# Optimization experiments

Measured on AMD Instinct MI355X. Metric: run time of the kernel, lower is better.

Reference implementation:

```python
import jax, jax.numpy as jnp
import numpy as np


def _chain_edges(n):
    # bidirectional chain edges + self loops (PyG GATConv add_self_loops=True default)
    src = np.concatenate([np.arange(n - 1), np.arange(1, n), np.arange(n)])
    dst = np.concatenate([np.arange(1, n), np.arange(n - 1), np.arange(n)])
    return jnp.asarray(src), jnp.asarray(dst)


def _gat(x, W, a_src, a_dst, bias, src, dst, n, heads, ch, concat):
    # x: [B, n, Fin]; PyG GATConv v1 math (lin has no bias, bias added post-agg)
    B = x.shape[0]
    xh = (x @ W).reshape(B, n, heads, ch)  # [B,n,h,c]
    es = jnp.einsum('bnhc,hc->bnh', xh, a_src)
    ed = jnp.einsum('bnhc,hc->bnh', xh, a_dst)
    e = jax.nn.leaky_relu(es[:, src] + ed[:, dst], 0.2)  # [B,E,h]
    e = jnp.moveaxis(e, 1, 0)                            # [E,B,h]
    m = jax.ops.segment_max(e, dst, num_segments=n)      # scatter-softmax over incoming edges
    w = jnp.exp(e - m[dst])
    denom = jax.ops.segment_sum(w, dst, num_segments=n)
    alpha = w / denom[dst]                               # [E,B,h]
    msgs = alpha[..., None] * jnp.moveaxis(xh[:, src], 1, 0)  # [E,B,h,c]
    out = jnp.moveaxis(jax.ops.segment_sum(msgs, dst, num_segments=n), 0, 1)  # [B,n,h,c]
    out = out.reshape(B, n, heads * ch) if concat else out.mean(axis=2)
    return out + bias


def _mlp(x, w1, b1, w2, b2, w3, b3):
    h = jax.nn.leaky_relu(x @ w1 + b1, 0.01)
    h = jax.nn.leaky_relu(h @ w2 + b2, 0.01)
    return h @ w3 + b3


def setup_inputs() -> dict:
    key = jax.random.key(0)
    ks = jax.random.split(key, 21)
    B, n, d_state, hid, da = 2048, 50, 64, 128, 4
    r = lambda k, shp, s: (jax.random.normal(k, shp, dtype=jnp.float32) * s)
    return {
        'state': r(ks[0], (B, n, d_state), 1.0),
        'W1': r(ks[1], (d_state, 2 * hid), 0.1), 'att_src1': r(ks[2], (2, hid), 0.1),
        'att_dst1': r(ks[3], (2, hid), 0.1), 'b1': r(ks[4], (2 * hid,), 0.02),
        'W2': r(ks[5], (2 * hid, hid), 0.1), 'att_src2': r(ks[6], (1, hid), 0.1),
        'att_dst2': r(ks[7], (1, hid), 0.1), 'b2': r(ks[8], (hid,), 0.02),
        'aw1': r(ks[9], (hid, 128), 0.1), 'ab1': r(ks[10], (128,), 0.02),
        'aw2': r(ks[11], (128, 128), 0.1), 'ab2': r(ks[12], (128,), 0.02),
        'aw3': r(ks[13], (128, da), 0.1), 'ab3': r(ks[14], (da,), 0.02),
        'vw1': r(ks[15], (hid, 128), 0.1), 'vb1': r(ks[16], (128,), 0.02),
        'vw2': r(ks[17], (128, 128), 0.1), 'vb2': r(ks[18], (128,), 0.02),
        'vw3': r(ks[19], (128, 1), 0.1), 'vb3': r(ks[20], (1,), 0.02),
    }


def reference(state, W1, att_src1, att_dst1, b1, W2, att_src2, att_dst2, b2,
              aw1, ab1, aw2, ab2, aw3, ab3, vw1, vb1, vw2, vb2, vw3, vb3):
    B, n, _ = state.shape
    src, dst = _chain_edges(n)
    x = jax.nn.gelu(_gat(state, W1, att_src1, att_dst1, b1, src, dst, n, 2, 128, True), approximate=False)
    x = jax.nn.gelu(_gat(x, W2, att_src2, att_dst2, b2, src, dst, n, 1, 128, False), approximate=False)
    graph_emb = x.mean(axis=1)                      # global_mean_pool over chain nodes
    value = _mlp(graph_emb, vw1, vb1, vw2, vb2, vw3, vb3)   # [B,1]
    mean = _mlp(x, aw1, ab1, aw2, ab2, aw3, ab3).reshape(B, -1)  # [B, n*d_action]
    return mean, value
```

## Files before the change

kernel.cpp:

```cpp
#include <hip/hip_runtime.h>

#define DI __device__ __forceinline__

typedef unsigned int uint32;
typedef unsigned short u16;
typedef __attribute__((ext_vector_type(8))) short s8v;
typedef __attribute__((ext_vector_type(4))) float f4v;

DI float lrelu(float x, float s){ return x > 0.f ? x : s*x; }
DI float fastrcp(float x){ float r; asm("v_rcp_f32 %0, %1" : "=v"(r) : "v"(x)); return r; }
DI u16 f2bu(float f){ uint32 u = __float_as_uint(f); return (u16)((u + 0x7FFFu + ((u>>16)&1u)) >> 16); }
DI float b16f(u16 u){ return __uint_as_float(((uint32)u)<<16); }

DI float gelu_f(float x){
  const float z = fabsf(x) * 0.70710678118654752f;
  const float t = fastrcp(1.f + 0.3275911f*z);
  float p = 1.061405429f;
  p = p*t - 1.453152027f;
  p = p*t + 1.421413741f;
  p = p*t - 0.284496736f;
  p = p*t + 0.254829592f;
  p = p*t;
  const float e = __expf(-z*z);
  float er = 1.f - p*e;
  er = copysignf(er, x);
  return 0.5f*x*(1.f + er);
}

DI f4v mfma16(s8v a, s8v b, f4v c){
  return __builtin_amdgcn_mfma_f32_16x16x32_bf16(a, b, c, 0, 0, 0);
}

constexpr int NNODE = 50;
constexpr int NT = 512;
constexpr int SCS = 134;

constexpr int WS1  = 0;
constexpr int WS2  = 18432;
constexpr int WSA1 = 55296;
constexpr int WSA2 = 71680;
constexpr int WSA3 = 88064;
constexpr int WSTOT= 90112;
constexpr int X2OFF= 90112;

__global__ __launch_bounds__(256)
void ac_prep(const float* __restrict__ w1, const float* __restrict__ as1, const float* __restrict__ ad1,
             const float* __restrict__ w2, const float* __restrict__ as2, const float* __restrict__ ad2,
             const float* __restrict__ aw1, const float* __restrict__ aw2, const float* __restrict__ aw3,
             u16* __restrict__ ws)
{
  const int T1 = 2*144*64, T2 = 144*256, T3 = 128*128;
  for (int t = blockIdx.x*blockDim.x + threadIdx.x; t < WSTOT; t += gridDim.x*blockDim.x){
    float v; int o;
    if (t < T1){
      int h = t / 9216, r = t - h*9216, n = r>>6, k = r&63;
      if (n < 128) v = w1[k*256 + h*128 + n];
      else if (n < 130){
        const float* av = ((n==129) ? ad1 : as1) + h*128;
        const float* wr = w1 + k*256 + h*128;
        float s = 0.f;
        for (int c=0;c<128;++c) s += wr[c]*av[c];
        v = s;
      } else v = 0.f;
      o = WS1 + h*9216 + n*64 + k;
    } else if (t < T1+T2){
      int j = t - T1, n = j>>8, k = j&255;
      if (n < 128) v = w2[k*128 + n];
      else if (n < 130){
        const float* av = (n==129) ? ad2 : as2;
        const float* wr = w2 + k*128;
        float s = 0.f;
        for (int c=0;c<128;++c) s += wr[c]*av[c];
        v = s;
      } else v = 0.f;
      o = WS2 + n*256 + k;
    } else if (t < T1+T2+T3){
      int j = t - T1 - T2, n = j>>7, k = j&127;
      v = aw1[k*128 + n];
      o = WSA1 + n*128 + k;
    } else if (t < T1+T2+2*T3){
      int j = t - T1 - T2 - T3, n = j>>7, k = j&127;
      v = aw2[k*128 + n];
      o = WSA2 + n*128 + k;
    } else {
      int j = t - T1 - T2 - 2*T3, m = j>>7, k = j&127;
      v = (m < 4) ? aw3[k*4 + m] : 0.f;
      o = WSA3 + m*128 + k;
    }
    ws[o] = f2bu(v);
  }
}

__global__ __launch_bounds__(NT)
void ac_gat(const float* __restrict__ state,
            const float* __restrict__ b1, const float* __restrict__ b2,
            u16* __restrict__ ws)
{
  __shared__ __align__(16) float sm[13100];
  u16*   pAb = (u16*)sm;
  u16*   pAs = (u16*)sm;
  float* sc  = sm + 6400;

  const int tid = threadIdx.x, b = blockIdx.x;
  const int wid = tid>>6, l15 = tid&15, g = (tid>>4)&3;

  {
    const float4* xb4 = (const float4*)(state + (size_t)b * (NNODE*64));
    for (int t = tid; t < 800; t += NT){
      float4 v = xb4[t];
      int i = t>>4, k0 = (t&15)*4;
      ushort4 u;
      u.x = f2bu(v.x); u.y = f2bu(v.y); u.z = f2bu(v.z); u.w = f2bu(v.w);
      *(ushort4*)(pAs + i*64 + (k0 ^ ((i&7)<<3))) = u;
    }
  }
  __syncthreads();

  s8v aS[4][2];
  #pragma unroll
  for (int mt=0;mt<4;++mt)
    #pragma unroll
    for (int ks=0;ks<2;++ks){
      int row = mt*16 + l15, c = ks*32 + g*8;
      aS[mt][ks] = *(const s8v*)(pAs + row*64 + (c ^ ((row&7)<<3)));
    }

  for (int h=0; h<2; ++h){
    for (int nt = wid; nt < 9; nt += 8){
      f4v acc[4];
      #pragma unroll
      for (int mt=0;mt<4;++mt) acc[mt] = (f4v){0.f,0.f,0.f,0.f};
      #pragma unroll
      for (int ks=0;ks<2;++ks){
        s8v bf = *(const s8v*)(ws + WS1 + h*9216 + (nt*16 + l15)*64 + ks*32 + g*8);
        #pragma unroll
        for (int mt=0;mt<4;++mt) acc[mt] = mfma16(aS[mt][ks], bf, acc[mt]);
      }
      const int col = nt*16 + l15;
      if (col < 130){
        #pragma unroll
        for (int mt=0;mt<4;++mt){
          #pragma unroll
          for (int r=0;r<4;++r){
            const int row = mt*16 + g*4 + r;
            if (mt < 3 || row < NNODE) sc[row*SCS + col] = acc[mt][r];
          }
        }
      }
    }
    __syncthreads();

    {
      const int i = tid & 63;
      if (i < NNODE){
        const float edi = sc[i*SCS + 129];
        const float eS = __expf(lrelu(sc[i*SCS + 128] + edi, 0.2f));
        const float eL = (i > 0)       ? __expf(lrelu(sc[(i-1)*SCS + 128] + edi, 0.2f)) : 0.f;
        const float eR = (i < NNODE-1) ? __expf(lrelu(sc[(i+1)*SCS + 128] + edi, 0.2f)) : 0.f;
        const float rs = fastrcp(eL + eS + eR);
        sc[i*SCS + 130] = eL*rs;
        sc[i*SCS + 131] = eS*rs;
        sc[i*SCS + 132] = eR*rs;
      }
    }
    {
      const int q = tid>>7, j = tid&127, jj = h*128 + j;
      const int i0 = q*13, i1 = (i0+13 < NNODE) ? i0+13 : NNODE;
      const float bj = b1[jj];
      float pv  = (i0 > 0) ? sc[(i0-1)*SCS + j] : 0.f;
      float cur = sc[i0*SCS + j];
      #pragma unroll 4
      for (int i = i0; i < i1; ++i){
        const float nx = (i < NNODE-1) ? sc[(i+1)*SCS + j] : 0.f;
        const float wL = sc[i*SCS + 130], wS = sc[i*SCS + 131], wR = sc[i*SCS + 132];
        const float v = gelu_f(wL*pv + wS*cur + wR*nx + bj);
        pAb[i*256 + (jj ^ ((i&7)<<3))] = f2bu(v);
        pv = cur; cur = nx;
      }
    }
    __syncthreads();
  }

  for (int nt = wid; nt < 9; nt += 8){
    f4v acc[4];
    #pragma unroll
    for (int mt=0;mt<4;++mt) acc[mt] = (f4v){0.f,0.f,0.f,0.f};
    #pragma unroll
    for (int ks=0;ks<8;++ks){
      s8v bf = *(const s8v*)(ws + WS2 + (nt*16 + l15)*256 + ks*32 + g*8);
      #pragma unroll
      for (int mt=0;mt<4;++mt){
        const int row = mt*16 + l15, c = ks*32 + g*8;
        s8v a = *(const s8v*)(pAb + row*256 + (c ^ ((row&7)<<3)));
        acc[mt] = mfma16(a, bf, acc[mt]);
      }
    }
    const int col = nt*16 + l15;
    if (col < 130){
      #pragma unroll
      for (int mt=0;mt<4;++mt){
        #pragma unroll
        for (int r=0;r<4;++r){
          const int row = mt*16 + g*4 + r;
          if (mt < 3 || row < NNODE) sc[row*SCS + col] = acc[mt][r];
        }
      }
    }
  }
  __syncthreads();

  {
    const int i = tid & 63;
    if (i < NNODE){
      const float edi = sc[i*SCS + 129];
      const float eS = __expf(lrelu(sc[i*SCS + 128] + edi, 0.2f));
      const float eL = (i > 0)       ? __expf(lrelu(sc[(i-1)*SCS + 128] + edi, 0.2f)) : 0.f;
      const float eR = (i < NNODE-1) ? __expf(lrelu(sc[(i+1)*SCS + 128] + edi, 0.2f)) : 0.f;
      const float rs = fastrcp(eL + eS + eR);
      sc[i*SCS + 130] = eL*rs;
      sc[i*SCS + 131] = eS*rs;
      sc[i*SCS + 132] = eR*rs;
    }
  }
  {
    u16* x2g = ws + X2OFF + (size_t)b * (NNODE*128);
    const int q = tid>>7, j = tid&127;
    const int i0 = q*13, i1 = (i0+13 < NNODE) ? i0+13 : NNODE;
    const float bj = b2[j];
    float pv  = (i0 > 0) ? sc[(i0-1)*SCS + j] : 0.f;
    float cur = sc[i0*SCS + j];
    #pragma unroll 4
    for (int i = i0; i < i1; ++i){
      const float nx = (i < NNODE-1) ? sc[(i+1)*SCS + j] : 0.f;
      const float wL = sc[i*SCS + 130], wS = sc[i*SCS + 131], wR = sc[i*SCS + 132];
      const float v = gelu_f(wL*pv + wS*cur + wR*nx + bj);
      x2g[i*128 + j] = f2bu(v);
      pv = cur; cur = nx;
    }
  }
}

__global__ __launch_bounds__(NT)
void ac_head(const u16* __restrict__ ws,
             const float* __restrict__ ab1, const float* __restrict__ ab2,
             const float* __restrict__ ab3, float* __restrict__ out_mean, int headM)
{
  __shared__ __align__(16) float sm[8192];
  u16* xt = (u16*)sm;
  u16* a4 = (u16*)(sm + 4096);

  const int tid = threadIdx.x, bid = blockIdx.x;
  const int wid = tid>>6, l15 = tid&15, g = (tid>>4)&3;

  {
    const int row = tid>>3, c0 = (tid&7)*16;
    const int grow = bid*64 + row;
    if (grow < headM){
      const uint4* src = (const uint4*)(ws + X2OFF + (size_t)grow*128 + c0);
      uint4 v0 = src[0], v1 = src[1];
      *(uint4*)(xt + row*128 + ( c0      ^ ((row&7)<<3))) = v0;
      *(uint4*)(xt + row*128 + ((c0 + 8) ^ ((row&7)<<3))) = v1;
    }
  }
  __syncthreads();

  {
    const int nt = wid;
    f4v acc[4];
    #pragma unroll
    for (int mt=0;mt<4;++mt) acc[mt] = (f4v){0.f,0.f,0.f,0.f};
    #pragma unroll
    for (int ks=0;ks<4;++ks){
      s8v bf = *(const s8v*)(ws + WSA1 + (nt*16 + l15)*128 + ks*32 + g*8);
      #pragma unroll
      for (int mt=0;mt<4;++mt){
        const int row = mt*16 + l15, c = ks*32 + g*8;
        s8v a = *(const s8v*)(xt + row*128 + (c ^ ((row&7)<<3)));
        acc[mt] = mfma16(a, bf, acc[mt]);
      }
    }
    const int col = nt*16 + l15;
    const float bj = ab1[col];
    #pragma unroll
    for (int mt=0;mt<4;++mt)
      #pragma unroll
      for (int r=0;r<4;++r){
        const int row = mt*16 + g*4 + r;
        a4[row*128 + (col ^ ((row&7)<<3))] = f2bu(lrelu(acc[mt][r] + bj, 0.01f));
      }
  }
  __syncthreads();

  {
    const int nt = wid;
    f4v acc[4];
    #pragma unroll
    for (int mt=0;mt<4;++mt) acc[mt] = (f4v){0.f,0.f,0.f,0.f};
    #pragma unroll
    for (int ks=0;ks<4;++ks){
      s8v bf = *(const s8v*)(ws + WSA2 + (nt*16 + l15)*128 + ks*32 + g*8);
      #pragma unroll
      for (int mt=0;mt<4;++mt){
        const int row = mt*16 + l15, c = ks*32 + g*8;
        s8v a = *(const s8v*)(a4 + row*128 + (c ^ ((row&7)<<3)));
        acc[mt] = mfma16(a, bf, acc[mt]);
      }
    }
    const int col = nt*16 + l15;
    const float bj = ab2[col];
    #pragma unroll
    for (int mt=0;mt<4;++mt)
      #pragma unroll
      for (int r=0;r<4;++r){
        const int row = mt*16 + g*4 + r;
        xt[row*128 + (col ^ ((row&7)<<3))] = f2bu(lrelu(acc[mt][r] + bj, 0.01f));
      }
  }
  __syncthreads();

  if (wid < 4){
    const int mt = wid;
    f4v acc = (f4v){0.f,0.f,0.f,0.f};
    #pragma unroll
    for (int ks=0;ks<4;++ks){
      s8v bf = *(const s8v*)(ws + WSA3 + l15*128 + ks*32 + g*8);
      const int row = mt*16 + l15, c = ks*32 + g*8;
      s8v a = *(const s8v*)(xt + row*128 + (c ^ ((row&7)<<3)));
      acc = mfma16(a, bf, acc);
    }
    if (l15 < 4){
      const float bj = ab3[l15];
      #pragma unroll
      for (int r=0;r<4;++r){
        const int grow = bid*64 + mt*16 + g*4 + r;
        if (grow < headM) out_mean[(size_t)grow*4 + l15] = acc[r] + bj;
      }
    }
  }
}

__global__ __launch_bounds__(NT)
void ac_value(const u16* __restrict__ ws,
              const float* __restrict__ vw1, const float* __restrict__ vb1,
              const float* __restrict__ vw2, const float* __restrict__ vb2,
              const float* __restrict__ vw3, const float* __restrict__ vb3,
              float* __restrict__ out_val, int B)
{
  __shared__ float gs[8*128];
  __shared__ float vs[8*128];
  const int tid = threadIdx.x, wid = tid>>6, j = tid&63;
  const int b = blockIdx.x*8 + wid;
  if (b >= B) return;
  const u16* xb = ws + X2OFF + (size_t)b * (NNODE*128);

  float g0 = 0.f, g1 = 0.f;
  for (int i=0;i<NNODE;++i){
    g0 += b16f(xb[i*128 + j]);
    g1 += b16f(xb[i*128 + 64 + j]);
  }
  gs[wid*128 + j]      = g0 * 0.02f;
  gs[wid*128 + 64 + j] = g1 * 0.02f;
  asm volatile("s_waitcnt lgkmcnt(0)" ::: "memory");
  __builtin_amdgcn_sched_barrier(0);

  float a0=0.f, a1=0.f;
  #pragma unroll 4
  for (int k=0;k<128;++k){
    const float gk = gs[wid*128 + k];
    a0 += gk*vw1[k*128 + j];
    a1 += gk*vw1[k*128 + j + 64];
  }
  vs[wid*128 + j]      = lrelu(a0 + vb1[j],    0.01f);
  vs[wid*128 + 64 + j] = lrelu(a1 + vb1[j+64], 0.01f);
  asm volatile("s_waitcnt lgkmcnt(0)" ::: "memory");
  __builtin_amdgcn_sched_barrier(0);

  float c0=0.f, c1=0.f;
  #pragma unroll 4
  for (int k=0;k<128;++k){
    const float hk = vs[wid*128 + k];
    c0 += hk*vw2[k*128 + j];
    c1 += hk*vw2[k*128 + j + 64];
  }
  const float va = lrelu(c0 + vb2[j],    0.01f);
  const float vb = lrelu(c1 + vb2[j+64], 0.01f);
  float p = va*vw3[j] + vb*vw3[j+64];
  #pragma unroll
  for (int off=32; off>0; off>>=1) p += __shfl_down(p, off);
  if (j == 0) out_val[b] = p + vb3[0];
}

__global__ __launch_bounds__(NT)
void ac_main(const float* __restrict__ state,
             const float* __restrict__ b1, const float* __restrict__ b2,
             const float* __restrict__ ab1, const float* __restrict__ ab2,
             const float* __restrict__ ab3,
             const float* __restrict__ vw1, const float* __restrict__ vb1,
             const float* __restrict__ vw2, const float* __restrict__ vb2,
             const float* __restrict__ vw3, const float* __restrict__ vb3,
             const u16* __restrict__ ws,
             float* __restrict__ out_mean, float* __restrict__ out_val)
{
  __shared__ __align__(16) float sm[13228];
  u16*   pAb  = (u16*)sm;
  u16*   pAs  = (u16*)sm;
  float* gebP = sm + 3200;
  float* vh1  = sm + 3712;
  float* sc   = sm + 6400;
  u16*   pAb2 = (u16*)(sm + 6400);
  float* geb  = sm + 13100;

  const int tid = threadIdx.x, b = blockIdx.x;
  const int wid = tid>>6, l15 = tid&15, g = (tid>>4)&3;

  {
    const float4* xb4 = (const float4*)(state + (size_t)b * (NNODE*64));
    for (int t = tid; t < 800; t += NT){
      float4 v = xb4[t];
      int i = t>>4, k0 = (t&15)*4;
      ushort4 u;
      u.x = f2bu(v.x); u.y = f2bu(v.y); u.z = f2bu(v.z); u.w = f2bu(v.w);
      *(ushort4*)(pAs + i*64 + (k0 ^ ((i&7)<<3))) = u;
    }
  }
  __syncthreads();

  s8v aS[4][2];
  #pragma unroll
  for (int mt=0;mt<4;++mt)
    #pragma unroll
    for (int ks=0;ks<2;++ks){
      int row = mt*16 + l15, c = ks*32 + g*8;
      aS[mt][ks] = *(const s8v*)(pAs + row*64 + (c ^ ((row&7)<<3)));
    }

  for (int h=0; h<2; ++h){
    for (int nt = wid; nt < 9; nt += 8){
      f4v acc[4];
      #pragma unroll
      for (int mt=0;mt<4;++mt) acc[mt] = (f4v){0.f,0.f,0.f,0.f};
      #pragma unroll
      for (int ks=0;ks<2;++ks){
        s8v bf = *(const s8v*)(ws + WS1 + h*9216 + (nt*16 + l15)*64 + ks*32 + g*8);
        #pragma unroll
        for (int mt=0;mt<4;++mt) acc[mt] = mfma16(aS[mt][ks], bf, acc[mt]);
      }
      const int col = nt*16 + l15;
      if (col < 130){
        #pragma unroll
        for (int mt=0;mt<4;++mt){
          #pragma unroll
          for (int r=0;r<4;++r){
            const int row = mt*16 + g*4 + r;
            if (mt < 3 || row < NNODE) sc[row*SCS + col] = acc[mt][r];
          }
        }
      }
    }
    __syncthreads();
    {
      const int i = tid & 63;
      if (i < NNODE){
        const float edi = sc[i*SCS + 129];
        const float eS = __expf(lrelu(sc[i*SCS + 128] + edi, 0.2f));
        const float eL = (i > 0)       ? __expf(lrelu(sc[(i-1)*SCS + 128] + edi, 0.2f)) : 0.f;
        const float eR = (i < NNODE-1) ? __expf(lrelu(sc[(i+1)*SCS + 128] + edi, 0.2f)) : 0.f;
        const float rs = fastrcp(eL + eS + eR);
        sc[i*SCS + 130] = eL*rs;
        sc[i*SCS + 131] = eS*rs;
        sc[i*SCS + 132] = eR*rs;
      }
    }
    {
      const int q = tid>>7, j = tid&127, jj = h*128 + j;
      const int i0 = q*13, i1 = (i0+13 < NNODE) ? i0+13 : NNODE;
      const float bj = b1[jj];
      float pv  = (i0 > 0) ? sc[(i0-1)*SCS + j] : 0.f;
      float cur = sc[i0*SCS + j];
      #pragma unroll 4
      for (int i = i0; i < i1; ++i){
        const float nx = (i < NNODE-1) ? sc[(i+1)*SCS + j] : 0.f;
        const float wL = sc[i*SCS + 130], wS = sc[i*SCS + 131], wR = sc[i*SCS + 132];
        const float v = gelu_f(wL*pv + wS*cur + wR*nx + bj);
        pAb[i*256 + (jj ^ ((i&7)<<3))] = f2bu(v);
        pv = cur; cur = nx;
      }
    }
    __syncthreads();
  }

  for (int nt = wid; nt < 9; nt += 8){
    f4v acc[4];
    #pragma unroll
    for (int mt=0;mt<4;++mt) acc[mt] = (f4v){0.f,0.f,0.f,0.f};
    #pragma unroll
    for (int ks=0;ks<8;++ks){
      s8v bf = *(const s8v*)(ws + WS2 + (nt*16 + l15)*256 + ks*32 + g*8);
      #pragma unroll
      for (int mt=0;mt<4;++mt){
        const int row = mt*16 + l15, c = ks*32 + g*8;
        s8v a = *(const s8v*)(pAb + row*256 + (c ^ ((row&7)<<3)));
        acc[mt] = mfma16(a, bf, acc[mt]);
      }
    }
    const int col = nt*16 + l15;
    if (col < 130){
      #pragma unroll
      for (int mt=0;mt<4;++mt){
        #pragma unroll
        for (int r=0;r<4;++r){
          const int row = mt*16 + g*4 + r;
          if (mt < 3 || row < NNODE) sc[row*SCS + col] = acc[mt][r];
        }
      }
    }
  }
  __syncthreads();

  {
    const int i = tid & 63;
    if (i < NNODE){
      const float edi = sc[i*SCS + 129];
      const float eS = __expf(lrelu(sc[i*SCS + 128] + edi, 0.2f));
      const float eL = (i > 0)       ? __expf(lrelu(sc[(i-1)*SCS + 128] + edi, 0.2f)) : 0.f;
      const float eR = (i < NNODE-1) ? __expf(lrelu(sc[(i+1)*SCS + 128] + edi, 0.2f)) : 0.f;
      const float rs = fastrcp(eL + eS + eR);
      sc[i*SCS + 130] = eL*rs;
      sc[i*SCS + 131] = eS*rs;
      sc[i*SCS + 132] = eR*rs;
    }
  }
  {
    const int q = tid>>7, j = tid&127;
    const int i0 = q*13, i1 = (i0+13 < NNODE) ? i0+13 : NNODE;
    const float bj = b2[j];
    float ps = 0.f;
    float pv  = (i0 > 0) ? sc[(i0-1)*SCS + j] : 0.f;
    float cur = sc[i0*SCS + j];
    #pragma unroll 4
    for (int i = i0; i < i1; ++i){
      const float nx = (i < NNODE-1) ? sc[(i+1)*SCS + j] : 0.f;
      const float wL = sc[i*SCS + 130], wS = sc[i*SCS + 131], wR = sc[i*SCS + 132];
      const float v = gelu_f(wL*pv + wS*cur + wR*nx + bj);
      pAb[i*128 + (j ^ ((i&7)<<3))] = f2bu(v);
      ps += v;
      pv = cur; cur = nx;
    }
    gebP[q*128 + j] = ps;
  }
  __syncthreads();

  {
    const int nt = wid;
    f4v acc[4];
    #pragma unroll
    for (int mt=0;mt<4;++mt) acc[mt] = (f4v){0.f,0.f,0.f,0.f};
    #pragma unroll
    for (int ks=0;ks<4;++ks){
      s8v bf = *(const s8v*)(ws + WSA1 + (nt*16 + l15)*128 + ks*32 + g*8);
      #pragma unroll
      for (int mt=0;mt<4;++mt){
        const int row = mt*16 + l15, c = ks*32 + g*8;
        s8v a = *(const s8v*)(pAb + row*128 + (c ^ ((row&7)<<3)));
        acc[mt] = mfma16(a, bf, acc[mt]);
      }
    }
    const int col = nt*16 + l15;
    const float bj = ab1[col];
    #pragma unroll
    for (int mt=0;mt<4;++mt){
      #pragma unroll
      for (int r=0;r<4;++r){
        const int row = mt*16 + g*4 + r;
        if (mt < 3 || row < NNODE){
          const float v = lrelu(acc[mt][r] + bj, 0.01f);
          pAb2[row*128 + (col ^ ((row&7)<<3))] = f2bu(v);
        }
      }
    }
    if (tid < 128)
      geb[tid] = (gebP[tid] + gebP[128+tid] + gebP[256+tid] + gebP[384+tid]) * 0.02f;
  }
  __syncthreads();

  {
    const int nt = wid;
    f4v acc[4];
    #pragma unroll
    for (int mt=0;mt<4;++mt) acc[mt] = (f4v){0.f,0.f,0.f,0.f};
    #pragma unroll
    for (int ks=0;ks<4;++ks){
      s8v bf = *(const s8v*)(ws + WSA2 + (nt*16 + l15)*128 + ks*32 + g*8);
      #pragma unroll
      for (int mt=0;mt<4;++mt){
        const int row = mt*16 + l15, c = ks*32 + g*8;
        s8v a = *(const s8v*)(pAb2 + row*128 + (c ^ ((row&7)<<3)));
        acc[mt] = mfma16(a, bf, acc[mt]);
      }
    }
    const int col = nt*16 + l15;
    const float bj = ab2[col];
    #pragma unroll
    for (int mt=0;mt<4;++mt){
      #pragma unroll
      for (int r=0;r<4;++r){
        const int row = mt*16 + g*4 + r;
        if (mt < 3 || row < NNODE){
          const float v = lrelu(acc[mt][r] + bj, 0.01f);
          pAb[row*128 + (col ^ ((row&7)<<3))] = f2bu(v);
        }
      }
    }
  }
  __syncthreads();

  if (wid < 4){
    const int mt = wid;
    f4v acc = (f4v){0.f,0.f,0.f,0.f};
    #pragma unroll
    for (int ks=0;ks<4;++ks){
      s8v bf = *(const s8v*)(ws + WSA3 + l15*128 + ks*32 + g*8);
      const int row = mt*16 + l15, c = ks*32 + g*8;
      s8v a = *(const s8v*)(pAb + row*128 + (c ^ ((row&7)<<3)));
      acc = mfma16(a, bf, acc);
    }
    if (l15 < 4){
      const float bj = ab3[l15];
      #pragma unroll
      for (int r=0;r<4;++r){
        const int row = mt*16 + g*4 + r;
        if (row < NNODE) out_mean[(size_t)b*200 + row*4 + l15] = acc[r] + bj;
      }
    }
  } else if (wid == 4){
    const int j = tid & 63;
    float a0=0.f, a1=0.f;
    #pragma unroll 4
    for (int k=0;k<128;++k){
      const float gk = geb[k];
      a0 += gk*vw1[k*128 + j];
      a1 += gk*vw1[k*128 + j + 64];
    }
    vh1[j]      = lrelu(a0 + vb1[j],    0.01f);
    vh1[j + 64] = lrelu(a1 + vb1[j+64], 0.01f);
    asm volatile("s_waitcnt lgkmcnt(0)" ::: "memory");
    __builtin_amdgcn_sched_barrier(0);
    float c0=0.f, c1=0.f;
    #pragma unroll 4
    for (int k=0;k<128;++k){
      const float hk = vh1[k];
      c0 += hk*vw2[k*128 + j];
      c1 += hk*vw2[k*128 + j + 64];
    }
    const float va = lrelu(c0 + vb2[j],    0.01f);
    const float vb = lrelu(c1 + vb2[j+64], 0.01f);
    float p = va*vw3[j] + vb*vw3[j+64];
    #pragma unroll
    for (int off=32; off>0; off>>=1) p += __shfl_down(p, off);
    if (j == 0) out_val[b] = p + vb3[0];
  }
}

extern "C" void kernel_launch(void* const* d_in, const int* in_sizes, int n_in,
                              void* d_out, int out_size, void* d_ws, size_t ws_size,
                              hipStream_t stream)
{
  const float* state = (const float*)d_in[0];
  const float* w1    = (const float*)d_in[1];
  const float* as1   = (const float*)d_in[2];
  const float* ad1   = (const float*)d_in[3];
  const float* b1_   = (const float*)d_in[4];
  const float* w2    = (const float*)d_in[5];
  const float* as2   = (const float*)d_in[6];
  const float* ad2   = (const float*)d_in[7];
  const float* b2_   = (const float*)d_in[8];
  const float* aw1   = (const float*)d_in[9];
  const float* ab1   = (const float*)d_in[10];
  const float* ab2   = (const float*)d_in[12];
  const float* aw2   = (const float*)d_in[11];
  const float* aw3   = (const float*)d_in[13];
  const float* ab3   = (const float*)d_in[14];
  const float* vw1   = (const float*)d_in[15];
  const float* vb1   = (const float*)d_in[16];
  const float* vw2   = (const float*)d_in[17];
  const float* vb2   = (const float*)d_in[18];
  const float* vw3   = (const float*)d_in[19];
  const float* vb3   = (const float*)d_in[20];

  const int B = in_sizes[0] / (NNODE * 64);
  float* out_mean = (float*)d_out;
  float* out_val  = out_mean + (size_t)B * 200;
  u16* ws = (u16*)d_ws;

  const size_t need = ((size_t)X2OFF + (size_t)B * NNODE * 128) * 2;

  ac_prep<<<128, 256, 0, stream>>>(w1, as1, ad1, w2, as2, ad2, aw1, aw2, aw3, ws);

  if (ws_size >= need){
    const int headM = B * NNODE;
    ac_gat<<<B, NT, 0, stream>>>(state, b1_, b2_, ws);
    ac_head<<<(headM + 63)/64, NT, 0, stream>>>(ws, ab1, ab2, ab3, out_mean, headM);
    ac_value<<<(B + 7)/8, NT, 0, stream>>>(ws, vw1, vb1, vw2, vb2, vw3, vb3, out_val, B);
  } else {
    ac_main<<<B, NT, 0, stream>>>(state, b1_, b2_, ab1, ab2, ab3,
                                  vw1, vb1, vw2, vb2, vw3, vb3,
                                  ws, out_mean, out_val);
  }
}
```

Baseline: 151.7 us.

## Fuse mean-pool into GAT kernel and merge head and value kernels

The GAT kernel now accumulates per-graph node sums of the layer-2 output in fp32 and writes the pooled embedding to a workspace buffer. The value MLP no longer re-reads the bf16 node features from global memory. The action-head and value kernels are merged into one launch whose block index selects the branch, removing one kernel launch and letting the value blocks overlap with the head blocks. This costs an extra block barrier in the GAT kernel and a larger workspace requirement. The pooled sum also now comes from fp32 values instead of bf16-rounded ones.

After: 153.2 us. No clear change (+1.0%).

```diff
diff --git a/kernel.cpp b/kernel.cpp
--- a/kernel.cpp
+++ b/kernel.cpp
@@ -94,11 +94,12 @@
 __global__ __launch_bounds__(NT)
 void ac_gat(const float* __restrict__ state,
             const float* __restrict__ b1, const float* __restrict__ b2,
-            u16* __restrict__ ws)
+            u16* __restrict__ ws, float* __restrict__ gebg)
 {
   __shared__ __align__(16) float sm[13100];
   u16*   pAb = (u16*)sm;
   u16*   pAs = (u16*)sm;
+  float* gebP = sm;
   float* sc  = sm + 6400;
 
   const int tid = threadIdx.x, b = blockIdx.x;
@@ -227,6 +228,7 @@
     const int q = tid>>7, j = tid&127;
     const int i0 = q*13, i1 = (i0+13 < NNODE) ? i0+13 : NNODE;
     const float bj = b2[j];
+    float ps = 0.f;
     float pv  = (i0 > 0) ? sc[(i0-1)*SCS + j] : 0.f;
     float cur = sc[i0*SCS + j];
     #pragma unroll 4
@@ -235,159 +237,160 @@
       const float wL = sc[i*SCS + 130], wS = sc[i*SCS + 131], wR = sc[i*SCS + 132];
       const float v = gelu_f(wL*pv + wS*cur + wR*nx + bj);
       x2g[i*128 + j] = f2bu(v);
+      ps += v;
       pv = cur; cur = nx;
     }
-  }
+    gebP[q*128 + j] = ps;
+  }
+  __syncthreads();
+  if (tid < 128)
+    gebg[(size_t)b*128 + tid] =
+      (gebP[tid] + gebP[128+tid] + gebP[256+tid] + gebP[384+tid]) * 0.02f;
 }
 
 __global__ __launch_bounds__(NT)
-void ac_head(const u16* __restrict__ ws,
+void ac_tail(const u16* __restrict__ ws,
              const float* __restrict__ ab1, const float* __restrict__ ab2,
-             const float* __restrict__ ab3, float* __restrict__ out_mean, int headM)
+             const float* __restrict__ ab3,
+             const float* __restrict__ vw1, const float* __restrict__ vb1,
+             const float* __restrict__ vw2, const float* __restrict__ vb2,
+             const float* __restrict__ vw3, const float* __restrict__ vb3,
+             const float* __restrict__ gebg,
+             float* __restrict__ out_mean, float* __restrict__ out_val,
+             int headM, int headBlocks, int B)
 {
   __shared__ __align__(16) float sm[8192];
-  u16* xt = (u16*)sm;
-  u16* a4 = (u16*)(sm + 4096);
-
-  const int tid = threadIdx.x, bid = blockIdx.x;
+  const int tid = threadIdx.x;
   const int wid = tid>>6, l15 = tid&15, g = (tid>>4)&3;
 
-  {
-    const int row = tid>>3, c0 = (tid&7)*16;
-    const int grow = bid*64 + row;
-    if (grow < headM){
-      const uint4* src = (const uint4*)(ws + X2OFF + (size_t)grow*128 + c0);
-      uint4 v0 = src[0], v1 = src[1];
-      *(uint4*)(xt + row*128 + ( c0      ^ ((row&7)<<3))) = v0;
-      *(uint4*)(xt + row*128 + ((c0 + 8) ^ ((row&7)<<3))) = v1;
-    }
-  }
-  __syncthreads();
-
-  {
-    const int nt = wid;
-    f4v acc[4];
-    #pragma unroll
-    for (int mt=0;mt<4;++mt) acc[mt] = (f4v){0.f,0.f,0.f,0.f};
-    #pragma unroll
-    for (int ks=0;ks<4;++ks){
-      s8v bf = *(const s8v*)(ws + WSA1 + (nt*16 + l15)*128 + ks*32 + g*8);
-      #pragma unroll
-      for (int mt=0;mt<4;++mt){
+  if ((int)blockIdx.x < headBlocks){
+    u16* xt = (u16*)sm;
+    u16* a4 = (u16*)(sm + 4096);
+    const int bid = blockIdx.x;
+
+    {
+      const int row = tid>>3, c0 = (tid&7)*16;
+      const int grow = bid*64 + row;
+      if (grow < headM){
+        const uint4* src = (const uint4*)(ws + X2OFF + (size_t)grow*128 + c0);
+        uint4 v0 = src[0], v1 = src[1];
+        *(uint4*)(xt + row*128 + ( c0      ^ ((row&7)<<3))) = v0;
+        *(uint4*)(xt + row*128 + ((c0 + 8) ^ ((row&7)<<3))) = v1;
+      }
+    }
+    __syncthreads();
+
+    {
+      const int nt = wid;
+      f4v acc[4];
+      #pragma unroll
+      for (int mt=0;mt<4;++mt) acc[mt] = (f4v){0.f,0.f,0.f,0.f};
+      #pragma unroll
+      for (int ks=0;ks<4;++ks){
+        s8v bf = *(const s8v*)(ws + WSA1 + (nt*16 + l15)*128 + ks*32 + g*8);
+        #pragma unroll
+        for (int mt=0;mt<4;++mt){
+          const int row = mt*16 + l15, c = ks*32 + g*8;
+          s8v a = *(const s8v*)(xt + row*128 + (c ^ ((row&7)<<3)));
+          acc[mt] = mfma16(a, bf, acc[mt]);
+        }
+      }
+      const int col = nt*16 + l15;
+      const float bj = ab1[col];
+      #pragma unroll
+      for (int mt=0;mt<4;++mt)
+        #pragma unroll
+        for (int r=0;r<4;++r){
+          const int row = mt*16 + g*4 + r;
+          a4[row*128 + (col ^ ((row&7)<<3))] = f2bu(lrelu(acc[mt][r] + bj, 0.01f));
+        }
+    }
+    __syncthreads();
+
+    {
+      const int nt = wid;
+      f4v acc[4];
+      #pragma unroll
+      for (int mt=0;mt<4;++mt) acc[mt] = (f4v){0.f,0.f,0.f,0.f};
+      #pragma unroll
+      for (int ks=0;ks<4;++ks){
+        s8v bf = *(const s8v*)(ws + WSA2 + (nt*16 + l15)*128 + ks*32 + g*8);
+        #pragma unroll
+        for (int mt=0;mt<4;++mt){
+          const int row = mt*16 + l15, c = ks*32 + g*8;
+          s8v a = *(const s8v*)(a4 + row*128 + (c ^ ((row&7)<<3)));
+          acc[mt] = mfma16(a, bf, acc[mt]);
+        }
+      }
+      const int col = nt*16 + l15;
+      const float bj = ab2[col];
+      #pragma unroll
+      for (int mt=0;mt<4;++mt)
+        #pragma unroll
+        for (int r=0;r<4;++r){
+          const int row = mt*16 + g*4 + r;
+          xt[row*128 + (col ^ ((row&7)<<3))] = f2bu(lrelu(acc[mt][r] + bj, 0.01f));
+        }
+    }
+    __syncthreads();
+
+    if (wid < 4){
+      const int mt = wid;
+      f4v acc = (f4v){0.f,0.f,0.f,0.f};
+      #pragma unroll
+      for (int ks=0;ks<4;++ks){
+        s8v bf = *(const s8v*)(ws + WSA3 + l15*128 + ks*32 + g*8);
         const int row = mt*16 + l15, c = ks*32 + g*8;
         s8v a = *(const s8v*)(xt + row*128 + (c ^ ((row&7)<<3)));
-        acc[mt] = mfma16(a, bf, acc[mt]);
-      }
-    }
-    const int col = nt*16 + l15;
-    const float bj = ab1[col];
-    #pragma unroll
-    for (int mt=0;mt<4;++mt)
-      #pragma unroll
-      for (int r=0;r<4;++r){
-        const int row = mt*16 + g*4 + r;
-        a4[row*128 + (col ^ ((row&7)<<3))] = f2bu(lrelu(acc[mt][r] + bj, 0.01f));
-      }
-  }
-  __syncthreads();
-
-  {
-    const int nt = wid;
-    f4v acc[4];
-    #pragma unroll
-    for (int mt=0;mt<4;++mt) acc[mt] = (f4v){0.f,0.f,0.f,0.f};
-    #pragma unroll
-    for (int ks=0;ks<4;++ks){
-      s8v bf = *(const s8v*)(ws + WSA2 + (nt*16 + l15)*128 + ks*32 + g*8);
-      #pragma unroll
-      for (int mt=0;mt<4;++mt){
-        const int row = mt*16 + l15, c = ks*32 + g*8;
-        s8v a = *(const s8v*)(a4 + row*128 + (c ^ ((row&7)<<3)));
-        acc[mt] = mfma16(a, bf, acc[mt]);
-      }
-    }
-    const int col = nt*16 + l15;
-    const float bj = ab2[col];
-    #pragma unroll
-    for (int mt=0;mt<4;++mt)
-      #pragma unroll
-      for (int r=0;r<4;++r){
-        const int row = mt*16 + g*4 + r;
-        xt[row*128 + (col ^ ((row&7)<<3))] = f2bu(lrelu(acc[mt][r] + bj, 0.01f));
-      }
-  }
-  __syncthreads();
-
-  if (wid < 4){
-    const int mt = wid;
-    f4v acc = (f4v){0.f,0.f,0.f,0.f};
-    #pragma unroll
-    for (int ks=0;ks<4;++ks){
-      s8v bf = *(const s8v*)(ws + WSA3 + l15*128 + ks*32 + g*8);
-      const int row = mt*16 + l15, c = ks*32 + g*8;
-      s8v a = *(const s8v*)(xt + row*128 + (c ^ ((row&7)<<3)));
-      acc = mfma16(a, bf, acc);
-    }
-    if (l15 < 4){
-      const float bj = ab3[l15];
-      #pragma unroll
-      for (int r=0;r<4;++r){
-        const int grow = bid*64 + mt*16 + g*4 + r;
-        if (grow < headM) out_mean[(size_t)grow*4 + l15] = acc[r] + bj;
-      }
-    }
-  }
-}
-
-__global__ __launch_bounds__(NT)
-void ac_value(const u16* __restrict__ ws,
-              const float* __restrict__ vw1, const float* __restrict__ vb1,
-              const float* __restrict__ vw2, const float* __restrict__ vb2,
-              const float* __restrict__ vw3, const float* __restrict__ vb3,
-              float* __restrict__ out_val, int B)
-{
-  __shared__ float gs[8*128];
-  __shared__ float vs[8*128];
-  const int tid = threadIdx.x, wid = tid>>6, j = tid&63;
-  const int b = blockIdx.x*8 + wid;
-  if (b >= B) return;
-  const u16* xb = ws + X2OFF + (size_t)b * (NNODE*128);
-
-  float g0 = 0.f, g1 = 0.f;
-  for (int i=0;i<NNODE;++i){
-    g0 += b16f(xb[i*128 + j]);
-    g1 += b16f(xb[i*128 + 64 + j]);
-  }
-  gs[wid*128 + j]      = g0 * 0.02f;
-  gs[wid*128 + 64 + j] = g1 * 0.02f;
-  asm volatile("s_waitcnt lgkmcnt(0)" ::: "memory");
-  __builtin_amdgcn_sched_barrier(0);
-
-  float a0=0.f, a1=0.f;
-  #pragma unroll 4
-  for (int k=0;k<128;++k){
-    const float gk = gs[wid*128 + k];
-    a0 += gk*vw1[k*128 + j];
-    a1 += gk*vw1[k*128 + j + 64];
-  }
-  vs[wid*128 + j]      = lrelu(a0 + vb1[j],    0.01f);
-  vs[wid*128 + 64 + j] = lrelu(a1 + vb1[j+64], 0.01f);
-  asm volatile("s_waitcnt lgkmcnt(0)" ::: "memory");
-  __builtin_amdgcn_sched_barrier(0);
-
-  float c0=0.f, c1=0.f;
-  #pragma unroll 4
-  for (int k=0;k<128;++k){
-    const float hk = vs[wid*128 + k];
-    c0 += hk*vw2[k*128 + j];
-    c1 += hk*vw2[k*128 + j + 64];
-  }
-  const float va = lrelu(c0 + vb2[j],    0.01f);
-  const float vb = lrelu(c1 + vb2[j+64], 0.01f);
-  float p = va*vw3[j] + vb*vw3[j+64];
-  #pragma unroll
-  for (int off=32; off>0; off>>=1) p += __shfl_down(p, off);
-  if (j == 0) out_val[b] = p + vb3[0];
+        acc = mfma16(a, bf, acc);
+      }
+      if (l15 < 4){
+        const float bj = ab3[l15];
+        #pragma unroll
+        for (int r=0;r<4;++r){
+          const int grow = bid*64 + mt*16 + g*4 + r;
+          if (grow < headM) out_mean[(size_t)grow*4 + l15] = acc[r] + bj;
+        }
+      }
+    }
+  } else {
+    const int j = tid & 63;
+    const int b = ((int)blockIdx.x - headBlocks)*8 + wid;
+    if (b >= B) return;
+    float* gw = sm + wid*128;
+    float* vs = sm + 1024 + wid*128;
+
+    gw[j]      = gebg[(size_t)b*128 + j];
+    gw[64 + j] = gebg[(size_t)b*128 + 64 + j];
+    asm volatile("s_waitcnt lgkmcnt(0)" ::: "memory");
+    __builtin_amdgcn_sched_barrier(0);
+
+    float a0=0.f, a1=0.f;
+    #pragma unroll 4
+    for (int k=0;k<128;++k){
+      const float gk = gw[k];
+      a0 += gk*vw1[k*128 + j];
+      a1 += gk*vw1[k*128 + j + 64];
+    }
+    vs[j]      = lrelu(a0 + vb1[j],    0.01f);
+    vs[64 + j] = lrelu(a1 + vb1[j+64], 0.01f);
+    asm volatile("s_waitcnt lgkmcnt(0)" ::: "memory");
+    __builtin_amdgcn_sched_barrier(0);
+
+    float c0=0.f, c1=0.f;
+    #pragma unroll 4
+    for (int k=0;k<128;++k){
+      const float hk = vs[k];
+      c0 += hk*vw2[k*128 + j];
+      c1 += hk*vw2[k*128 + j + 64];
+    }
+    const float va = lrelu(c0 + vb2[j],    0.01f);
+    const float vb = lrelu(c1 + vb2[j+64], 0.01f);
+    float p = va*vw3[j] + vb*vw3[j+64];
+    #pragma unroll
+    for (int off=32; off>0; off>>=1) p += __shfl_down(p, off);
+    if (j == 0) out_val[b] = p + vb3[0];
+  }
 }
 
 __global__ __launch_bounds__(NT)
@@ -676,8 +679,8 @@
   const float* b2_   = (const float*)d_in[8];
   const float* aw1   = (const float*)d_in[9];
   const float* ab1   = (const float*)d_in[10];
+  const float* aw2   = (const float*)d_in[11];
   const float* ab2   = (const float*)d_in[12];
-  const float* aw2   = (const float*)d_in[11];
   const float* aw3   = (const float*)d_in[13];
   const float* ab3   = (const float*)d_in[14];
   const float* vw1   = (const float*)d_in[15];
@@ -692,15 +695,20 @@
   float* out_val  = out_mean + (size_t)B * 200;
   u16* ws = (u16*)d_ws;
 
-  const size_t need = ((size_t)X2OFF + (size_t)B * NNODE * 128) * 2;
+  const size_t x2_u16  = (size_t)B * NNODE * 128;
+  const size_t geb_off = (size_t)X2OFF + x2_u16;
+  const size_t need    = geb_off*2 + (size_t)B*128*4;
 
   ac_prep<<<128, 256, 0, stream>>>(w1, as1, ad1, w2, as2, ad2, aw1, aw2, aw3, ws);
 
   if (ws_size >= need){
+    float* gebg = (float*)(ws + geb_off);
     const int headM = B * NNODE;
-    ac_gat<<<B, NT, 0, stream>>>(state, b1_, b2_, ws);
-    ac_head<<<(headM + 63)/64, NT, 0, stream>>>(ws, ab1, ab2, ab3, out_mean, headM);
-    ac_value<<<(B + 7)/8, NT, 0, stream>>>(ws, vw1, vb1, vw2, vb2, vw3, vb3, out_val, B);
+    const int headBlocks = (headM + 63)/64;
+    const int valBlocks  = (B + 7)/8;
+    ac_gat<<<B, NT, 0, stream>>>(state, b1_, b2_, ws, gebg);
+    ac_tail<<<headBlocks + valBlocks, NT, 0, stream>>>(ws, ab1, ab2, ab3,
+        vw1, vb1, vw2, vb2, vw3, vb3, gebg, out_mean, out_val, headM, headBlocks, B);
   } else {
     ac_main<<<B, NT, 0, stream>>>(state, b1_, b2_, ab1, ab2, ab3,
                                   vw1, vb1, vw2, vb2, vw3, vb3,
```
